# Kernel optimization log

Measured on AMD Instinct MI355X. Metric: run time of the kernel, lower is better.

The kernel has to match this reference:

```python
import jax, jax.numpy as jnp
import numpy as np

N = 100000      # nodes (categories_nums[0])
E = 1600000     # edges
FEAT = 16       # features_num
HID = 32        # hidden
IDE = 16        # id_embed_size
EMB = 8         # embed_size
CAT_MAX = 1000  # categorical vocab (categories_nums[1:])
K = 3           # TAGConv hops (sparse=False)
NC = 2          # num_class
IN_DIM = IDE + 2 * EMB + HID  # 64 -> TAGConv input
EPS = 1e-5


def layer_norm(x, g, b):
    m = jnp.mean(x, axis=-1, keepdims=True)
    v = jnp.mean((x - m) ** 2, axis=-1, keepdims=True)
    return (x - m) * jax.lax.rsqrt(v + EPS) * g + b


def setup_inputs() -> dict:
    key = jax.random.key(0)
    ks = jax.random.split(key, 20)
    s = 0.05
    return {
        "x": jax.random.normal(ks[0], (N, FEAT), jnp.float32),
        "edge_index": jax.random.randint(ks[1], (2, E), 0, N, jnp.int64),
        "edge_weight": jax.random.uniform(ks[2], (E,), jnp.float32),
        "categories_value": jax.random.randint(ks[3], (N, 3), 0, CAT_MAX, jnp.int64),
        "id_table": jax.random.normal(ks[4], (N, IDE), jnp.float32) * s,
        "lin0_id_W": jax.random.normal(ks[5], (IDE, IDE), jnp.float32) * s,
        "lin0_id_b": jnp.zeros((IDE,), jnp.float32),
        "emb1": jax.random.normal(ks[6], (CAT_MAX, EMB), jnp.float32) * s,
        "emb2": jax.random.normal(ks[7], (CAT_MAX, EMB), jnp.float32) * s,
        "lin0_emb_W": jax.random.normal(ks[8], (2 * EMB, 2 * EMB), jnp.float32) * s,
        "lin0_emb_b": jnp.zeros((2 * EMB,), jnp.float32),
        "lin0_W": jax.random.normal(ks[9], (FEAT, HID), jnp.float32) * s,
        "lin0_b": jnp.zeros((HID,), jnp.float32),
        "ln0_g": jnp.ones((IN_DIM,), jnp.float32),
        "ln0_b": jnp.zeros((IN_DIM,), jnp.float32),
        "tag_W": jax.random.normal(ks[10], (K + 1, IN_DIM, HID), jnp.float32) * s,
        "tag_b": jnp.zeros((HID,), jnp.float32),
        "ln1_g": jnp.ones((HID,), jnp.float32),
        "ln1_b": jnp.zeros((HID,), jnp.float32),
        "lin1_W": jax.random.normal(ks[11], (HID, NC), jnp.float32) * s,
        "lin1_b": jnp.zeros((NC,), jnp.float32),
    }


def reference(x, edge_index, edge_weight, categories_value, id_table, lin0_id_W,
              lin0_id_b, emb1, emb2, lin0_emb_W, lin0_emb_b, lin0_W, lin0_b,
              ln0_g, ln0_b, tag_W, tag_b, ln1_g, ln1_b, lin1_W, lin1_b):
    # eval mode: dropouts are identity
    h = jax.nn.elu(x @ lin0_W + lin0_b)                       # [N, HID]
    ide = id_table[categories_value[:, 0]]                    # [N, IDE]
    ide = jax.nn.elu(ide @ lin0_id_W + lin0_id_b)
    er = jnp.concatenate([emb1[categories_value[:, 1]],
                          emb2[categories_value[:, 2]]], axis=1)  # [N, 2*EMB]
    er = jax.nn.elu(er @ lin0_emb_W + lin0_emb_b)
    feat = jnp.concatenate([ide, h, er], axis=1)              # [N, IN_DIM]
    feat = layer_norm(feat, ln0_g, ln0_b)

    # TAGConv: gcn_norm without self-loops, K-hop propagation
    row, col = edge_index[0], edge_index[1]                   # source -> target
    deg = jax.ops.segment_sum(edge_weight, col, num_segments=N)
    dis = jnp.where(deg > 0, deg ** -0.5, 0.0)
    norm = dis[row] * edge_weight * dis[col]                  # [E]

    out = feat @ tag_W[0]                                     # [N, HID]
    xk = feat
    for k in range(1, K + 1):
        xk = jax.ops.segment_sum(xk[row] * norm[:, None], col, num_segments=N)
        out = out + xk @ tag_W[k]
    out = out + tag_b

    out = jax.nn.relu(out)
    out = layer_norm(out, ln1_g, ln1_b)
    out = out @ lin1_W + lin1_b                               # [N, NC]
    return jax.nn.log_softmax(out, axis=-1)
```

## Files before the change

kernel.cpp:

```cpp
#include <hip/hip_runtime.h>
#include <hip/hip_bf16.h>

typedef unsigned short u16;
typedef unsigned int   u32;
typedef unsigned long long u64;
typedef u32 u32x2 __attribute__((ext_vector_type(2)));
typedef u32 u32x4 __attribute__((ext_vector_type(4)));

#define FIX_SCALE 16777216.0f
#define FIX_INV   (1.0f / 16777216.0f)
#define CNT_SHIFT 40
#define DEG_MASK  ((1ULL << CNT_SHIFT) - 1)

__device__ __forceinline__ float b2f(u16 u) { return __uint_as_float(((u32)u) << 16); }
__device__ __forceinline__ u16 f2b(float f) {
    u32 u = __float_as_uint(f);
    return (u16)((u + 0x7FFFu + ((u >> 16) & 1u)) >> 16);
}
__device__ __forceinline__ float elu(float v) { return v > 0.f ? v : expm1f(v); }
__device__ __forceinline__ float ldf(const void* p, size_t i, int f32) {
    return f32 ? ((const float*)p)[i] : b2f(((const u16*)p)[i]);
}
__device__ __forceinline__ float plo(u32 a) { return __uint_as_float(a << 16); }
__device__ __forceinline__ float phi(u32 a) { return __uint_as_float(a & 0xFFFF0000u); }

__global__ void k_flags(const u32* __restrict__ gw, const int* __restrict__ ei,
                        const int* __restrict__ cat, int* __restrict__ flags) {
    if (threadIdx.x == 0 && blockIdx.x == 0) {
        flags[0] = (gw[0] == 0x3F800000u) ? 1 : 0;
        flags[1] = ((ei[1]  | ei[3]  | ei[5]  | ei[7])  == 0) ? 2 : 1;
        flags[2] = ((cat[1] | cat[3] | cat[5] | cat[7]) == 0) ? 2 : 1;
    }
}

__global__ __launch_bounds__(256) void k_feathist(
    const void* __restrict__ x, const int* __restrict__ cat,
    const void* __restrict__ id_table, const void* __restrict__ W_id, const void* __restrict__ b_id,
    const void* __restrict__ emb1, const void* __restrict__ emb2,
    const void* __restrict__ W_emb, const void* __restrict__ b_emb,
    const void* __restrict__ W0, const void* __restrict__ b0,
    const void* __restrict__ g0, const void* __restrict__ bb0,
    const void* __restrict__ tagW,
    float* __restrict__ out_acc, u32* __restrict__ z1, u32* __restrict__ z2, u32* __restrict__ z3,
    const int* __restrict__ ei, const void* __restrict__ ew,
    u64* __restrict__ packed, u16* __restrict__ rank,
    const int* __restrict__ flags, int N, int E, int nbN)
{
    __shared__ float sW0[512];
    __shared__ float sb0[32];
    __shared__ float sWid[256];
    __shared__ float sbid[16];
    __shared__ float sWe[256];
    __shared__ float sbe[16];
    __shared__ float sg[64], sb[64];
    __shared__ float sTt[8192];
    int tid = threadIdx.x;
    int f32 = flags[0], s = flags[1], cs = flags[2];

    int e0 = blockIdx.x * 512 + tid;
    int e1 = e0 + 256;
    u64 old0 = 0, old1 = 0;
    bool h0 = (e0 < E), h1 = (e1 < E);
    const int* colp = ei + (size_t)E * s;
    if (h0) {
        int cdst = colp[(size_t)e0 * s];
        float w = ldf(ew, e0, f32);
        old0 = atomicAdd(&packed[cdst], (1ULL << CNT_SHIFT) | (u64)(w * FIX_SCALE + 0.5f));
    }
    if (h1) {
        int cdst = colp[(size_t)e1 * s];
        float w = ldf(ew, e1, f32);
        old1 = atomicAdd(&packed[cdst], (1ULL << CNT_SHIFT) | (u64)(w * FIX_SCALE + 0.5f));
    }

    if (blockIdx.x < nbN) {
        for (int i = tid; i < 512; i += 256) sW0[i] = ldf(W0, i, f32);
        if (tid < 32) sb0[tid] = ldf(b0, tid, f32);
        sWid[tid] = ldf(W_id, tid, f32);
        if (tid < 16) sbid[tid] = ldf(b_id, tid, f32);
        sWe[tid] = ldf(W_emb, tid, f32);
        if (tid < 16) sbe[tid] = ldf(b_emb, tid, f32);
        if (tid < 64) { sg[tid] = ldf(g0, tid, f32); sb[tid] = ldf(bb0, tid, f32); }
        for (int i = tid; i < 8192; i += 256) {
            int k = i >> 11, r = i & 2047, j = r >> 6, d = r & 63;
            sTt[i] = ldf(tagW, (size_t)k * 2048 + (size_t)d * 32 + j, f32);
        }
        __syncthreads();

        int i = blockIdx.x * 256 + tid;
        if (i < N) {
            size_t cb = (size_t)i * 3 * cs;
            int c0 = cat[cb], c1 = cat[cb + cs], c2 = cat[cb + 2 * cs];
            float f[64];
            {
                float t[16];
                #pragma unroll
                for (int q = 0; q < 16; q++) t[q] = ldf(id_table, (size_t)c0 * 16 + q, f32);
                #pragma unroll
                for (int j = 0; j < 16; j++) {
                    float a = sbid[j];
                    #pragma unroll
                    for (int ff = 0; ff < 16; ff++) a += t[ff] * sWid[ff * 16 + j];
                    f[j] = elu(a);
                }
            }
            {
                float t[16];
                #pragma unroll
                for (int q = 0; q < 16; q++) t[q] = ldf(x, (size_t)i * 16 + q, f32);
                #pragma unroll
                for (int j = 0; j < 32; j++) {
                    float a = sb0[j];
                    #pragma unroll
                    for (int ff = 0; ff < 16; ff++) a += t[ff] * sW0[ff * 32 + j];
                    f[16 + j] = elu(a);
                }
            }
            {
                float t[16];
                #pragma unroll
                for (int q = 0; q < 8; q++) t[q] = ldf(emb1, (size_t)c1 * 8 + q, f32);
                #pragma unroll
                for (int q = 0; q < 8; q++) t[8 + q] = ldf(emb2, (size_t)c2 * 8 + q, f32);
                #pragma unroll
                for (int j = 0; j < 16; j++) {
                    float a = sbe[j];
                    #pragma unroll
                    for (int ff = 0; ff < 16; ff++) a += t[ff] * sWe[ff * 16 + j];
                    f[48 + j] = elu(a);
                }
            }
            float m = 0.f;
            #pragma unroll
            for (int d = 0; d < 64; d++) m += f[d];
            m *= (1.f / 64.f);
            float var = 0.f;
            #pragma unroll
            for (int d = 0; d < 64; d++) { float df = f[d] - m; var += df * df; }
            var *= (1.f / 64.f);
            float rs = rsqrtf(var + 1e-5f);
            #pragma unroll
            for (int d = 0; d < 64; d++) f[d] = (f[d] - m) * rs * sg[d] + sb[d];

            float* oa = out_acc + (size_t)i * 32;
            for (int j = 0; j < 32; j++) {
                float a = 0.f;
                #pragma unroll
                for (int d = 0; d < 64; d++) a += f[d] * sTt[j * 64 + d];
                oa[j] = a;
            }
            #pragma unroll
            for (int k = 1; k <= 3; k++) {
                u32* zp = ((k == 1) ? z1 : (k == 2) ? z2 : z3) + (size_t)i * 16;
                const float* T = sTt + k * 2048;
                for (int j = 0; j < 16; j++) {
                    float a0 = 0.f, a1 = 0.f;
                    #pragma unroll
                    for (int d = 0; d < 64; d++) {
                        a0 += f[d] * T[(2 * j) * 64 + d];
                        a1 += f[d] * T[(2 * j + 1) * 64 + d];
                    }
                    zp[j] = ((u32)f2b(a1) << 16) | f2b(a0);
                }
            }
        }
    }
    if (h0) rank[e0] = (u16)(old0 >> CNT_SHIFT);
    if (h1) rank[e1] = (u16)(old1 >> CNT_SHIFT);
}

__global__ __launch_bounds__(256) void k_scan1(const u64* __restrict__ packed, int* __restrict__ ebuf,
                                               int* __restrict__ bsum, float* __restrict__ dis, int N)
{
    __shared__ int sdat[256];
    int tid = threadIdx.x;
    int i = blockIdx.x * 256 + tid;
    u64 pv = (i < N) ? packed[i] : 0ULL;
    int v = (int)(pv >> CNT_SHIFT);
    sdat[tid] = v;
    __syncthreads();
    for (int off = 1; off < 256; off <<= 1) {
        int t = (tid >= off) ? sdat[tid - off] : 0;
        __syncthreads();
        sdat[tid] += t;
        __syncthreads();
    }
    if (i < N) {
        ebuf[i] = sdat[tid] - v;
        u64 db = pv & DEG_MASK;
        dis[i] = db ? rsqrtf((float)db * FIX_INV) : 0.f;
    }
    if (tid == 255) bsum[blockIdx.x] = sdat[255];
}

__global__ __launch_bounds__(512) void k_scan2(const int* __restrict__ bsum, int* __restrict__ boff, int NB)
{
    __shared__ int sdat[512];
    __shared__ int scarry;
    int tid = threadIdx.x;
    if (tid == 0) scarry = 0;
    __syncthreads();
    for (int base = 0; base < NB; base += 512) {
        int i = base + tid;
        int v = (i < NB) ? bsum[i] : 0;
        sdat[tid] = v;
        __syncthreads();
        for (int off = 1; off < 512; off <<= 1) {
            int t = (tid >= off) ? sdat[tid - off] : 0;
            __syncthreads();
            sdat[tid] += t;
            __syncthreads();
        }
        if (i < NB) boff[i] = scarry + sdat[tid] - v;
        __syncthreads();
        if (tid == 0) scarry += sdat[511];
        __syncthreads();
    }
}

__global__ __launch_bounds__(256) void k_scan3(const int* __restrict__ ebuf, const int* __restrict__ boff,
                                               int* __restrict__ rowptr, int N, int E)
{
    int i = blockIdx.x * 256 + threadIdx.x;
    if (i >= N) return;
    rowptr[i] = boff[blockIdx.x] + ebuf[i];
    if (i == N - 1) rowptr[N] = E;
}

__global__ __launch_bounds__(256) void k_scatter(const int* __restrict__ ei, const void* __restrict__ ew,
                                                 const float* __restrict__ dis, const u16* __restrict__ rank,
                                                 const int* __restrict__ rowptr, int2* __restrict__ csr,
                                                 const int* __restrict__ flags, int E)
{
    int f32 = flags[0], s = flags[1];
    const int* row = ei;
    const int* col = ei + (size_t)E * s;
    int e = blockIdx.x * 256 + threadIdx.x;
    if (e >= E) return;
    int r = row[(size_t)e * s], c = col[(size_t)e * s];
    float nrm = dis[r] * ldf(ew, e, f32) * dis[c];
    csr[rowptr[c] + (int)rank[e]] = make_int2(r, __float_as_int(nrm));
}

template<int ADD>
__global__ __launch_bounds__(256) void k_ahop(
    const u32* __restrict__ zin, const u32* __restrict__ zadd, u32* __restrict__ uout,
    const int* __restrict__ rowptr, const int2* __restrict__ csr, int N)
{
    int tid = threadIdx.x;
    int node = blockIdx.x * 4 + (tid >> 6);
    if (node >= N) return;
    int lane = tid & 63;
    int o = (lane >> 3) & 7;
    int c = lane & 7;
    int start = rowptr[node], end = rowptr[node + 1];

    const u32x2* fin2 = (const u32x2*)zin;
    float v0 = 0.f, v1 = 0.f, v2 = 0.f, v3 = 0.f;
    int e = start;
    for (; e + 16 <= end; e += 16) {
        int2 ma = csr[e + o];
        int2 mb = csr[e + 8 + o];
        u32x2 aa = fin2[(size_t)(u32)ma.x * 8 + c];
        u32x2 ab = fin2[(size_t)(u32)mb.x * 8 + c];
        float wa = __int_as_float(ma.y), wb = __int_as_float(mb.y);
        v0 += plo(aa.x) * wa; v1 += phi(aa.x) * wa; v2 += plo(aa.y) * wa; v3 += phi(aa.y) * wa;
        v0 += plo(ab.x) * wb; v1 += phi(ab.x) * wb; v2 += plo(ab.y) * wb; v3 += phi(ab.y) * wb;
    }
    for (; e < end; e += 8) {
        int ee = e + o;
        int2 m = (ee < end) ? csr[ee] : make_int2(0, 0);
        u32x2 a = fin2[(size_t)(u32)m.x * 8 + c];
        float w = __int_as_float(m.y);
        v0 += plo(a.x) * w; v1 += phi(a.x) * w; v2 += plo(a.y) * w; v3 += phi(a.y) * w;
    }
    v0 += __shfl_xor(v0, 8);  v1 += __shfl_xor(v1, 8);  v2 += __shfl_xor(v2, 8);  v3 += __shfl_xor(v3, 8);
    v0 += __shfl_xor(v0, 16); v1 += __shfl_xor(v1, 16); v2 += __shfl_xor(v2, 16); v3 += __shfl_xor(v3, 16);
    v0 += __shfl_xor(v0, 32); v1 += __shfl_xor(v1, 32); v2 += __shfl_xor(v2, 32); v3 += __shfl_xor(v3, 32);

    if (lane < 8) {
        if (ADD) {
            u32x2 z = ((const u32x2*)zadd)[(size_t)node * 8 + lane];
            v0 += plo(z.x); v1 += phi(z.x); v2 += plo(z.y); v3 += phi(z.y);
        }
        u32x2 pw;
        pw.x = ((u32)f2b(v1) << 16) | f2b(v0);
        pw.y = ((u32)f2b(v3) << 16) | f2b(v2);
        ((u32x2*)uout)[(size_t)node * 8 + lane] = pw;
    }
}

__global__ __launch_bounds__(256) void k_head(
    const float* __restrict__ oacc, const u32* __restrict__ t1,
    const void* __restrict__ tag_b,
    const void* __restrict__ g1, const void* __restrict__ b1,
    const void* __restrict__ W1, const void* __restrict__ bb1,
    void* __restrict__ out, const int* __restrict__ flags, int N)
{
    __shared__ float stb[32], sg[32], sbb[32], sW1[64], sb1v[2];
    int tid = threadIdx.x;
    int f32 = flags[0];
    if (tid < 32) { stb[tid] = ldf(tag_b, tid, f32); sg[tid] = ldf(g1, tid, f32); sbb[tid] = ldf(b1, tid, f32); }
    if (tid < 64) sW1[tid] = ldf(W1, tid, f32);
    if (tid < 2) sb1v[tid] = ldf(bb1, tid, f32);
    __syncthreads();

    int i = blockIdx.x * 256 + tid;
    if (i >= N) return;

    float acc[32];
    const float4* oa4 = (const float4*)(oacc + (size_t)i * 32);
    #pragma unroll
    for (int q = 0; q < 8; q++) {
        float4 t = oa4[q];
        acc[4 * q] = t.x; acc[4 * q + 1] = t.y; acc[4 * q + 2] = t.z; acc[4 * q + 3] = t.w;
    }
    const u32x2* tp = (const u32x2*)t1 + (size_t)i * 8;
    #pragma unroll
    for (int q = 0; q < 8; q++) {
        u32x2 z = tp[q];
        acc[4 * q]     += plo(z.x); acc[4 * q + 1] += phi(z.x);
        acc[4 * q + 2] += plo(z.y); acc[4 * q + 3] += phi(z.y);
    }
    float o[32]; float m = 0.f;
    #pragma unroll
    for (int j = 0; j < 32; j++) { float t = acc[j] + stb[j]; t = t > 0.f ? t : 0.f; o[j] = t; m += t; }
    m *= (1.f / 32.f);
    float var = 0.f;
    #pragma unroll
    for (int j = 0; j < 32; j++) { float d = o[j] - m; var += d * d; }
    var *= (1.f / 32.f);
    float rs = rsqrtf(var + 1e-5f);
    float z0 = sb1v[0], z1 = sb1v[1];
    #pragma unroll
    for (int j = 0; j < 32; j++) {
        float t = (o[j] - m) * rs * sg[j] + sbb[j];
        z0 += t * sW1[2 * j];
        z1 += t * sW1[2 * j + 1];
    }
    float mx = fmaxf(z0, z1);
    float l = mx + logf(expf(z0 - mx) + expf(z1 - mx));
    if (f32) {
        ((float*)out)[(size_t)i * 2]     = z0 - l;
        ((float*)out)[(size_t)i * 2 + 1] = z1 - l;
    } else {
        *((u32*)((u16*)out + (size_t)i * 2)) = ((u32)f2b(z1 - l) << 16) | f2b(z0 - l);
    }
}

extern "C" void kernel_launch(void* const* d_in, const int* in_sizes, int n_in,
                              void* d_out, int out_size, void* d_ws, size_t ws_size,
                              hipStream_t stream)
{
    const void* x        = d_in[0];
    const int*  ei       = (const int*)d_in[1];
    const void* ew       = d_in[2];
    const int*  cat      = (const int*)d_in[3];
    const void* id_table = d_in[4];
    const void* W_id     = d_in[5];
    const void* b_id     = d_in[6];
    const void* emb1     = d_in[7];
    const void* emb2     = d_in[8];
    const void* W_emb    = d_in[9];
    const void* b_emb    = d_in[10];
    const void* W0       = d_in[11];
    const void* b0       = d_in[12];
    const void* g0       = d_in[13];
    const void* bb0      = d_in[14];
    const void* tagW     = d_in[15];
    const void* tag_b    = d_in[16];
    const void* g1       = d_in[17];
    const void* b1       = d_in[18];
    const void* W1       = d_in[19];
    const void* bb1      = d_in[20];

    int N = in_sizes[0] / 16;
    int E = in_sizes[2];
    int nb = (N + 255) / 256;
    int eb = (E + 255) / 256;
    int eb2 = (E + 511) / 512;

    char* ws = (char*)d_ws;
    size_t off = 0;
    int*   flags  = (int*)(ws + off);   off += 256;
    float* oacc   = (float*)(ws + off); off += (size_t)N * 32 * 4;
    u32*   z1     = (u32*)(ws + off);   off += (size_t)N * 16 * 4;
    u32*   z2     = (u32*)(ws + off);   off += (size_t)N * 16 * 4;
    u32*   z3     = (u32*)(ws + off);   off += (size_t)N * 16 * 4;
    u32*   u2     = (u32*)(ws + off);   off += (size_t)N * 16 * 4;
    int2*  csr    = (int2*)(ws + off);  off += (size_t)E * 8;
    int*   rowptr = (int*)(ws + off);   off += ((size_t)N + 1) * 4;
    off = (off + 255) & ~(size_t)255;
    u16*   rank   = (u16*)(ws + off);   off += (size_t)E * 2;
    off = (off + 255) & ~(size_t)255;
    u64*   packed = (u64*)(ws + off);   off += (size_t)N * 8;
    int*   ebuf   = (int*)(ws + off);   off += (size_t)N * 4;
    float* dis    = (float*)(ws + off); off += (size_t)N * 4;
    int*   bsum   = (int*)(ws + off);   off += (size_t)nb * 4;
    int*   boff   = (int*)(ws + off);   off += (size_t)nb * 4;

    hipMemsetAsync(packed, 0, (size_t)N * 8, stream);
    k_flags<<<1, 64, 0, stream>>>((const u32*)g0, ei, cat, flags);

    k_feathist<<<eb2, 256, 0, stream>>>(x, cat, id_table, W_id, b_id, emb1, emb2, W_emb, b_emb,
                                        W0, b0, g0, bb0, tagW, oacc, z1, z2, z3,
                                        ei, ew, packed, rank, flags, N, E, nb);
    k_scan1<<<nb, 256, 0, stream>>>(packed, ebuf, bsum, dis, N);
    k_scan2<<<1, 512, 0, stream>>>(bsum, boff, nb);
    k_scan3<<<nb, 256, 0, stream>>>(ebuf, boff, rowptr, N, E);
    k_scatter<<<eb, 256, 0, stream>>>(ei, ew, dis, rank, rowptr, csr, flags, E);

    int hb = (N + 3) / 4;
    k_ahop<1><<<hb, 256, 0, stream>>>(z3, z2, u2, rowptr, csr, N);
    k_ahop<1><<<hb, 256, 0, stream>>>(u2, z1, z3, rowptr, csr, N);
    k_ahop<0><<<hb, 256, 0, stream>>>(z3, z1, z2, rowptr, csr, N);
    k_head<<<nb, 256, 0, stream>>>(oacc, z2, tag_b, g1, b1, W1, bb1, d_out, flags, N);
}
```

Measured before the change: 365.8 us.

## Split TAG weight projection out of feature kernel into parallel zproj kernel

The per-node 64x128 projection onto the four TAGConv weight matrices moves out of the fused feature/histogram kernel. That kernel now writes a bf16 normalized feature row. A new kernel spreads each node's projection across 8 threads, each handling one hop and one output half, with weights held in padded shared memory. This removes the 32KB shared weight tile and the serial per-thread 8192-FMA loop from the edge-histogram kernel, which should raise occupancy. The cost is an extra launch, an extra round-trip through the bf16 feature buffer, and bf16 rounding of the features before the projection.

Result: slower. 455.4 us (+24.5%).

```diff
diff --git a/kernel.cpp b/kernel.cpp
--- a/kernel.cpp
+++ b/kernel.cpp
@@ -40,8 +40,7 @@
     const void* __restrict__ W_emb, const void* __restrict__ b_emb,
     const void* __restrict__ W0, const void* __restrict__ b0,
     const void* __restrict__ g0, const void* __restrict__ bb0,
-    const void* __restrict__ tagW,
-    float* __restrict__ out_acc, u32* __restrict__ z1, u32* __restrict__ z2, u32* __restrict__ z3,
+    u32* __restrict__ feat,
     const int* __restrict__ ei, const void* __restrict__ ew,
     u64* __restrict__ packed, u16* __restrict__ rank,
     const int* __restrict__ flags, int N, int E, int nbN)
@@ -53,7 +52,6 @@
     __shared__ float sWe[256];
     __shared__ float sbe[16];
     __shared__ float sg[64], sb[64];
-    __shared__ float sTt[8192];
     int tid = threadIdx.x;
     int f32 = flags[0], s = flags[1], cs = flags[2];
 
@@ -81,10 +79,6 @@
         sWe[tid] = ldf(W_emb, tid, f32);
         if (tid < 16) sbe[tid] = ldf(b_emb, tid, f32);
         if (tid < 64) { sg[tid] = ldf(g0, tid, f32); sb[tid] = ldf(bb0, tid, f32); }
-        for (int i = tid; i < 8192; i += 256) {
-            int k = i >> 11, r = i & 2047, j = r >> 6, d = r & 63;
-            sTt[i] = ldf(tagW, (size_t)k * 2048 + (size_t)d * 32 + j, f32);
-        }
         __syncthreads();
 
         int i = blockIdx.x * 256 + tid;
@@ -142,31 +136,64 @@
             #pragma unroll
             for (int d = 0; d < 64; d++) f[d] = (f[d] - m) * rs * sg[d] + sb[d];
 
-            float* oa = out_acc + (size_t)i * 32;
-            for (int j = 0; j < 32; j++) {
-                float a = 0.f;
-                #pragma unroll
-                for (int d = 0; d < 64; d++) a += f[d] * sTt[j * 64 + d];
-                oa[j] = a;
-            }
+            u32* fp = feat + (size_t)i * 32;
             #pragma unroll
-            for (int k = 1; k <= 3; k++) {
-                u32* zp = ((k == 1) ? z1 : (k == 2) ? z2 : z3) + (size_t)i * 16;
-                const float* T = sTt + k * 2048;
-                for (int j = 0; j < 16; j++) {
-                    float a0 = 0.f, a1 = 0.f;
-                    #pragma unroll
-                    for (int d = 0; d < 64; d++) {
-                        a0 += f[d] * T[(2 * j) * 64 + d];
-                        a1 += f[d] * T[(2 * j + 1) * 64 + d];
-                    }
-                    zp[j] = ((u32)f2b(a1) << 16) | f2b(a0);
-                }
-            }
+            for (int q = 0; q < 32; q++) fp[q] = ((u32)f2b(f[2 * q + 1]) << 16) | f2b(f[2 * q]);
         }
     }
     if (h0) rank[e0] = (u16)(old0 >> CNT_SHIFT);
     if (h1) rank[e1] = (u16)(old1 >> CNT_SHIFT);
+}
+
+__global__ __launch_bounds__(256) void k_zproj(
+    const u32* __restrict__ feat, const void* __restrict__ tagW,
+    float* __restrict__ oacc, u32* __restrict__ z1, u32* __restrict__ z2, u32* __restrict__ z3,
+    const int* __restrict__ flags, int N)
+{
+    __shared__ float sT[4 * 2056];
+    int tid = threadIdx.x;
+    int f32 = flags[0];
+    for (int i = tid; i < 8192; i += 256) {
+        int k = i >> 11, r = i & 2047;
+        sT[k * 2056 + r] = ldf(tagW, i, f32);
+    }
+    __syncthreads();
+
+    int nblk = blockIdx.x * 32 + (tid >> 3);
+    if (nblk >= N) return;
+    int sub = tid & 7, kk = sub >> 1, h = sub & 1;
+
+    const u32x4* fp4 = (const u32x4*)(feat + (size_t)nblk * 32);
+    float f[64];
+    #pragma unroll
+    for (int q = 0; q < 8; q++) {
+        u32x4 a = fp4[q];
+        f[8 * q + 0] = plo(a.x); f[8 * q + 1] = phi(a.x);
+        f[8 * q + 2] = plo(a.y); f[8 * q + 3] = phi(a.y);
+        f[8 * q + 4] = plo(a.z); f[8 * q + 5] = phi(a.z);
+        f[8 * q + 6] = plo(a.w); f[8 * q + 7] = phi(a.w);
+    }
+
+    float o[16];
+    #pragma unroll
+    for (int j = 0; j < 16; j++) o[j] = 0.f;
+    const float* T = sT + kk * 2056 + h * 16;
+    #pragma unroll 4
+    for (int d = 0; d < 64; d++) {
+        float fd = f[d];
+        #pragma unroll
+        for (int j = 0; j < 16; j++) o[j] += fd * T[d * 32 + j];
+    }
+
+    if (kk == 0) {
+        float4* op = (float4*)(oacc + (size_t)nblk * 32 + h * 16);
+        #pragma unroll
+        for (int q = 0; q < 4; q++) op[q] = make_float4(o[4 * q], o[4 * q + 1], o[4 * q + 2], o[4 * q + 3]);
+    } else {
+        u32* zp = ((kk == 1) ? z1 : (kk == 2) ? z2 : z3) + (size_t)nblk * 16 + h * 8;
+        #pragma unroll
+        for (int jj = 0; jj < 8; jj++) zp[jj] = ((u32)f2b(o[2 * jj + 1]) << 16) | f2b(o[2 * jj]);
+    }
 }
 
 __global__ __launch_bounds__(256) void k_scan1(const u64* __restrict__ packed, int* __restrict__ ebuf,
@@ -379,11 +406,13 @@
     int nb = (N + 255) / 256;
     int eb = (E + 255) / 256;
     int eb2 = (E + 511) / 512;
+    int zb = (N + 31) / 32;
 
     char* ws = (char*)d_ws;
     size_t off = 0;
     int*   flags  = (int*)(ws + off);   off += 256;
     float* oacc   = (float*)(ws + off); off += (size_t)N * 32 * 4;
+    u32*   feat   = (u32*)(ws + off);   off += (size_t)N * 32 * 4;
     u32*   z1     = (u32*)(ws + off);   off += (size_t)N * 16 * 4;
     u32*   z2     = (u32*)(ws + off);   off += (size_t)N * 16 * 4;
     u32*   z3     = (u32*)(ws + off);   off += (size_t)N * 16 * 4;
@@ -403,8 +432,10 @@
     k_flags<<<1, 64, 0, stream>>>((const u32*)g0, ei, cat, flags);
 
     k_feathist<<<eb2, 256, 0, stream>>>(x, cat, id_table, W_id, b_id, emb1, emb2, W_emb, b_emb,
-                                        W0, b0, g0, bb0, tagW, oacc, z1, z2, z3,
+                                        W0, b0, g0, bb0, feat,
                                         ei, ew, packed, rank, flags, N, E, nb);
+    k_zproj<<<zb, 256, 0, stream>>>(feat, tagW, oacc, z1, z2, z3, flags, N);
+
     k_scan1<<<nb, 256, 0, stream>>>(packed, ebuf, bsum, dis, N);
     k_scan2<<<1, 512, 0, stream>>>(bsum, boff, nb);
     k_scan3<<<nb, 256, 0, stream>>>(ebuf, boff, rowptr, N, E);
```

## Rebalance fused feature/histogram kernel: 16 edges per thread, all blocks compute nodes

Applied to the files above, without the earlier changes.

The fused feature-transform and degree-histogram kernel now launches about as many blocks as node tiles, with each thread handling 16 edges instead of 2. All 16 edge atomics are issued together before the dense projection, so their latency can overlap with the matmul work. The TAG weight matrix is kept in its natural row layout, the projection is restructured as an outer product with 32 accumulators, and outputs are written with vector stores. In exchange, each thread holds many more live registers (f[64], o[32], 16 pending atomics), which may lower occupancy.

Measured after the change: 479.0 us. +31.0%, slower.

```diff
diff --git a/kernel.cpp b/kernel.cpp
--- a/kernel.cpp
+++ b/kernel.cpp
@@ -41,10 +41,10 @@
     const void* __restrict__ W0, const void* __restrict__ b0,
     const void* __restrict__ g0, const void* __restrict__ bb0,
     const void* __restrict__ tagW,
-    float* __restrict__ out_acc, u32* __restrict__ z1, u32* __restrict__ z2, u32* __restrict__ z3,
+    float* __restrict__ oacc, u32* __restrict__ z1, u32* __restrict__ z2, u32* __restrict__ z3,
     const int* __restrict__ ei, const void* __restrict__ ew,
     u64* __restrict__ packed, u16* __restrict__ rank,
-    const int* __restrict__ flags, int N, int E, int nbN)
+    const int* __restrict__ flags, int N, int E)
 {
     __shared__ float sW0[512];
     __shared__ float sb0[32];
@@ -53,120 +53,132 @@
     __shared__ float sWe[256];
     __shared__ float sbe[16];
     __shared__ float sg[64], sb[64];
-    __shared__ float sTt[8192];
+    __shared__ float sT[4 * 2048];
     int tid = threadIdx.x;
     int f32 = flags[0], s = flags[1], cs = flags[2];
 
-    int e0 = blockIdx.x * 512 + tid;
-    int e1 = e0 + 256;
-    u64 old0 = 0, old1 = 0;
-    bool h0 = (e0 < E), h1 = (e1 < E);
+    for (int i = tid; i < 512; i += 256) sW0[i] = ldf(W0, i, f32);
+    if (tid < 32) sb0[tid] = ldf(b0, tid, f32);
+    sWid[tid] = ldf(W_id, tid, f32);
+    if (tid < 16) sbid[tid] = ldf(b_id, tid, f32);
+    sWe[tid] = ldf(W_emb, tid, f32);
+    if (tid < 16) sbe[tid] = ldf(b_emb, tid, f32);
+    if (tid < 64) { sg[tid] = ldf(g0, tid, f32); sb[tid] = ldf(bb0, tid, f32); }
+    for (int i = tid; i < 8192; i += 256) sT[i] = ldf(tagW, i, f32);
+    __syncthreads();
+
+    int i = blockIdx.x * 256 + tid;
+    bool node = (i < N);
+    float f[64];
+    if (node) {
+        size_t cb = (size_t)i * 3 * cs;
+        int c0 = cat[cb], c1 = cat[cb + cs], c2 = cat[cb + 2 * cs];
+        {
+            float t[16];
+            #pragma unroll
+            for (int q = 0; q < 16; q++) t[q] = ldf(id_table, (size_t)c0 * 16 + q, f32);
+            #pragma unroll
+            for (int j = 0; j < 16; j++) {
+                float a = sbid[j];
+                #pragma unroll
+                for (int ff = 0; ff < 16; ff++) a += t[ff] * sWid[ff * 16 + j];
+                f[j] = elu(a);
+            }
+        }
+        {
+            float t[16];
+            #pragma unroll
+            for (int q = 0; q < 16; q++) t[q] = ldf(x, (size_t)i * 16 + q, f32);
+            #pragma unroll
+            for (int j = 0; j < 32; j++) {
+                float a = sb0[j];
+                #pragma unroll
+                for (int ff = 0; ff < 16; ff++) a += t[ff] * sW0[ff * 32 + j];
+                f[16 + j] = elu(a);
+            }
+        }
+        {
+            float t[16];
+            #pragma unroll
+            for (int q = 0; q < 8; q++) t[q] = ldf(emb1, (size_t)c1 * 8 + q, f32);
+            #pragma unroll
+            for (int q = 0; q < 8; q++) t[8 + q] = ldf(emb2, (size_t)c2 * 8 + q, f32);
+            #pragma unroll
+            for (int j = 0; j < 16; j++) {
+                float a = sbe[j];
+                #pragma unroll
+                for (int ff = 0; ff < 16; ff++) a += t[ff] * sWe[ff * 16 + j];
+                f[48 + j] = elu(a);
+            }
+        }
+        float m = 0.f;
+        #pragma unroll
+        for (int d = 0; d < 64; d++) m += f[d];
+        m *= (1.f / 64.f);
+        float var = 0.f;
+        #pragma unroll
+        for (int d = 0; d < 64; d++) { float df = f[d] - m; var += df * df; }
+        var *= (1.f / 64.f);
+        float rs = rsqrtf(var + 1e-5f);
+        #pragma unroll
+        for (int d = 0; d < 64; d++) f[d] = (f[d] - m) * rs * sg[d] + sb[d];
+    }
+
+    int ebase = blockIdx.x * 4096 + tid;
     const int* colp = ei + (size_t)E * s;
-    if (h0) {
-        int cdst = colp[(size_t)e0 * s];
-        float w = ldf(ew, e0, f32);
-        old0 = atomicAdd(&packed[cdst], (1ULL << CNT_SHIFT) | (u64)(w * FIX_SCALE + 0.5f));
-    }
-    if (h1) {
-        int cdst = colp[(size_t)e1 * s];
-        float w = ldf(ew, e1, f32);
-        old1 = atomicAdd(&packed[cdst], (1ULL << CNT_SHIFT) | (u64)(w * FIX_SCALE + 0.5f));
-    }
-
-    if (blockIdx.x < nbN) {
-        for (int i = tid; i < 512; i += 256) sW0[i] = ldf(W0, i, f32);
-        if (tid < 32) sb0[tid] = ldf(b0, tid, f32);
-        sWid[tid] = ldf(W_id, tid, f32);
-        if (tid < 16) sbid[tid] = ldf(b_id, tid, f32);
-        sWe[tid] = ldf(W_emb, tid, f32);
-        if (tid < 16) sbe[tid] = ldf(b_emb, tid, f32);
-        if (tid < 64) { sg[tid] = ldf(g0, tid, f32); sb[tid] = ldf(bb0, tid, f32); }
-        for (int i = tid; i < 8192; i += 256) {
-            int k = i >> 11, r = i & 2047, j = r >> 6, d = r & 63;
-            sTt[i] = ldf(tagW, (size_t)k * 2048 + (size_t)d * 32 + j, f32);
-        }
-        __syncthreads();
-
-        int i = blockIdx.x * 256 + tid;
-        if (i < N) {
-            size_t cb = (size_t)i * 3 * cs;
-            int c0 = cat[cb], c1 = cat[cb + cs], c2 = cat[cb + 2 * cs];
-            float f[64];
-            {
-                float t[16];
-                #pragma unroll
-                for (int q = 0; q < 16; q++) t[q] = ldf(id_table, (size_t)c0 * 16 + q, f32);
-                #pragma unroll
-                for (int j = 0; j < 16; j++) {
-                    float a = sbid[j];
-                    #pragma unroll
-                    for (int ff = 0; ff < 16; ff++) a += t[ff] * sWid[ff * 16 + j];
-                    f[j] = elu(a);
+    int cd[16]; float wv[16];
+    #pragma unroll
+    for (int k = 0; k < 16; k++) {
+        int e = ebase + (k << 8);
+        if (e < E) { cd[k] = colp[(size_t)e * s]; wv[k] = ldf(ew, e, f32); }
+    }
+    u64 olds[16];
+    #pragma unroll
+    for (int k = 0; k < 16; k++) {
+        int e = ebase + (k << 8);
+        if (e < E)
+            olds[k] = atomicAdd(&packed[cd[k]],
+                                (1ULL << CNT_SHIFT) | (u64)(wv[k] * FIX_SCALE + 0.5f));
+    }
+
+    if (node) {
+        #pragma unroll
+        for (int p = 0; p < 4; p++) {
+            float o[32];
+            #pragma unroll
+            for (int j = 0; j < 32; j++) o[j] = 0.f;
+            const float* T = sT + p * 2048;
+            #pragma unroll
+            for (int d = 0; d < 64; d++) {
+                float fd = f[d];
+                #pragma unroll
+                for (int j = 0; j < 32; j++) o[j] += fd * T[d * 32 + j];
+            }
+            if (p == 0) {
+                float4* op = (float4*)(oacc + (size_t)i * 32);
+                #pragma unroll
+                for (int q = 0; q < 8; q++)
+                    op[q] = make_float4(o[4 * q], o[4 * q + 1], o[4 * q + 2], o[4 * q + 3]);
+            } else {
+                u32* zp = ((p == 1) ? z1 : (p == 2) ? z2 : z3) + (size_t)i * 16;
+                #pragma unroll
+                for (int q = 0; q < 4; q++) {
+                    u32x4 pw;
+                    pw.x = ((u32)f2b(o[8 * q + 1]) << 16) | f2b(o[8 * q + 0]);
+                    pw.y = ((u32)f2b(o[8 * q + 3]) << 16) | f2b(o[8 * q + 2]);
+                    pw.z = ((u32)f2b(o[8 * q + 5]) << 16) | f2b(o[8 * q + 4]);
+                    pw.w = ((u32)f2b(o[8 * q + 7]) << 16) | f2b(o[8 * q + 6]);
+                    ((u32x4*)zp)[q] = pw;
                 }
             }
-            {
-                float t[16];
-                #pragma unroll
-                for (int q = 0; q < 16; q++) t[q] = ldf(x, (size_t)i * 16 + q, f32);
-                #pragma unroll
-                for (int j = 0; j < 32; j++) {
-                    float a = sb0[j];
-                    #pragma unroll
-                    for (int ff = 0; ff < 16; ff++) a += t[ff] * sW0[ff * 32 + j];
-                    f[16 + j] = elu(a);
-                }
-            }
-            {
-                float t[16];
-                #pragma unroll
-                for (int q = 0; q < 8; q++) t[q] = ldf(emb1, (size_t)c1 * 8 + q, f32);
-                #pragma unroll
-                for (int q = 0; q < 8; q++) t[8 + q] = ldf(emb2, (size_t)c2 * 8 + q, f32);
-                #pragma unroll
-                for (int j = 0; j < 16; j++) {
-                    float a = sbe[j];
-                    #pragma unroll
-                    for (int ff = 0; ff < 16; ff++) a += t[ff] * sWe[ff * 16 + j];
-                    f[48 + j] = elu(a);
-                }
-            }
-            float m = 0.f;
-            #pragma unroll
-            for (int d = 0; d < 64; d++) m += f[d];
-            m *= (1.f / 64.f);
-            float var = 0.f;
-            #pragma unroll
-            for (int d = 0; d < 64; d++) { float df = f[d] - m; var += df * df; }
-            var *= (1.f / 64.f);
-            float rs = rsqrtf(var + 1e-5f);
-            #pragma unroll
-            for (int d = 0; d < 64; d++) f[d] = (f[d] - m) * rs * sg[d] + sb[d];
-
-            float* oa = out_acc + (size_t)i * 32;
-            for (int j = 0; j < 32; j++) {
-                float a = 0.f;
-                #pragma unroll
-                for (int d = 0; d < 64; d++) a += f[d] * sTt[j * 64 + d];
-                oa[j] = a;
-            }
-            #pragma unroll
-            for (int k = 1; k <= 3; k++) {
-                u32* zp = ((k == 1) ? z1 : (k == 2) ? z2 : z3) + (size_t)i * 16;
-                const float* T = sTt + k * 2048;
-                for (int j = 0; j < 16; j++) {
-                    float a0 = 0.f, a1 = 0.f;
-                    #pragma unroll
-                    for (int d = 0; d < 64; d++) {
-                        a0 += f[d] * T[(2 * j) * 64 + d];
-                        a1 += f[d] * T[(2 * j + 1) * 64 + d];
-                    }
-                    zp[j] = ((u32)f2b(a1) << 16) | f2b(a0);
-                }
-            }
-        }
-    }
-    if (h0) rank[e0] = (u16)(old0 >> CNT_SHIFT);
-    if (h1) rank[e1] = (u16)(old1 >> CNT_SHIFT);
+        }
+    }
+
+    #pragma unroll
+    for (int k = 0; k < 16; k++) {
+        int e = ebase + (k << 8);
+        if (e < E) rank[e] = (u16)(olds[k] >> CNT_SHIFT);
+    }
 }
 
 __global__ __launch_bounds__(256) void k_scan1(const u64* __restrict__ packed, int* __restrict__ ebuf,
@@ -378,7 +390,8 @@
     int E = in_sizes[2];
     int nb = (N + 255) / 256;
     int eb = (E + 255) / 256;
-    int eb2 = (E + 511) / 512;
+    int fb = (E + 4095) / 4096;
+    if (fb < nb) fb = nb;
 
     char* ws = (char*)d_ws;
     size_t off = 0;
@@ -402,9 +415,10 @@
     hipMemsetAsync(packed, 0, (size_t)N * 8, stream);
     k_flags<<<1, 64, 0, stream>>>((const u32*)g0, ei, cat, flags);
 
-    k_feathist<<<eb2, 256, 0, stream>>>(x, cat, id_table, W_id, b_id, emb1, emb2, W_emb, b_emb,
-                                        W0, b0, g0, bb0, tagW, oacc, z1, z2, z3,
-                                        ei, ew, packed, rank, flags, N, E, nb);
+    k_feathist<<<fb, 256, 0, stream>>>(x, cat, id_table, W_id, b_id, emb1, emb2, W_emb, b_emb,
+                                       W0, b0, g0, bb0, tagW, oacc, z1, z2, z3,
+                                       ei, ew, packed, rank, flags, N, E);
+
     k_scan1<<<nb, 256, 0, stream>>>(packed, ebuf, bsum, dis, N);
     k_scan2<<<1, 512, 0, stream>>>(bsum, boff, nb);
     k_scan3<<<nb, 256, 0, stream>>>(ebuf, boff, rowptr, N, E);
```

## Split node feature work across 8 lanes per node with shuffle-based layernorm

Applied to the files above, without the earlier changes.

The fused feature/histogram kernel now processes 32 nodes per block with 8 threads per node instead of one thread per node over the first N/256 blocks. Inputs and embedding rows are staged in shared memory, layernorm statistics are reduced with warp shuffles, and each lane computes one 16-wide slice of one of the four TAG projections, writing vectorized stores. This spreads the heavy per-node 64x128 matmul across all edge blocks instead of a few threads, reducing register pressure and serialization. In exchange, every block reloads the full 8K weight table into shared memory and the matmul issues many lane shuffles.

Result: slower. 395.5 us (+8.1%).

```diff
diff --git a/kernel.cpp b/kernel.cpp
--- a/kernel.cpp
+++ b/kernel.cpp
@@ -41,130 +41,169 @@
     const void* __restrict__ W0, const void* __restrict__ b0,
     const void* __restrict__ g0, const void* __restrict__ bb0,
     const void* __restrict__ tagW,
-    float* __restrict__ out_acc, u32* __restrict__ z1, u32* __restrict__ z2, u32* __restrict__ z3,
+    float* __restrict__ oacc, u32* __restrict__ z1, u32* __restrict__ z2, u32* __restrict__ z3,
     const int* __restrict__ ei, const void* __restrict__ ew,
     u64* __restrict__ packed, u16* __restrict__ rank,
-    const int* __restrict__ flags, int N, int E, int nbN)
+    const int* __restrict__ flags, int N, int E)
 {
     __shared__ float sW0[512];
-    __shared__ float sb0[32];
+    __shared__ float sb0v[32];
     __shared__ float sWid[256];
     __shared__ float sbid[16];
     __shared__ float sWe[256];
     __shared__ float sbe[16];
     __shared__ float sg[64], sb[64];
-    __shared__ float sTt[8192];
+    __shared__ float sT[4 * 2056];
+    __shared__ float sx[32 * 17];
+    __shared__ float sid[32 * 17];
+    __shared__ float se[32 * 17];
+    __shared__ int   scat[96];
     int tid = threadIdx.x;
     int f32 = flags[0], s = flags[1], cs = flags[2];
 
     int e0 = blockIdx.x * 512 + tid;
     int e1 = e0 + 256;
-    u64 old0 = 0, old1 = 0;
     bool h0 = (e0 < E), h1 = (e1 < E);
     const int* colp = ei + (size_t)E * s;
-    if (h0) {
-        int cdst = colp[(size_t)e0 * s];
-        float w = ldf(ew, e0, f32);
-        old0 = atomicAdd(&packed[cdst], (1ULL << CNT_SHIFT) | (u64)(w * FIX_SCALE + 0.5f));
-    }
-    if (h1) {
-        int cdst = colp[(size_t)e1 * s];
-        float w = ldf(ew, e1, f32);
-        old1 = atomicAdd(&packed[cdst], (1ULL << CNT_SHIFT) | (u64)(w * FIX_SCALE + 0.5f));
-    }
-
-    if (blockIdx.x < nbN) {
-        for (int i = tid; i < 512; i += 256) sW0[i] = ldf(W0, i, f32);
-        if (tid < 32) sb0[tid] = ldf(b0, tid, f32);
-        sWid[tid] = ldf(W_id, tid, f32);
-        if (tid < 16) sbid[tid] = ldf(b_id, tid, f32);
-        sWe[tid] = ldf(W_emb, tid, f32);
-        if (tid < 16) sbe[tid] = ldf(b_emb, tid, f32);
-        if (tid < 64) { sg[tid] = ldf(g0, tid, f32); sb[tid] = ldf(bb0, tid, f32); }
-        for (int i = tid; i < 8192; i += 256) {
-            int k = i >> 11, r = i & 2047, j = r >> 6, d = r & 63;
-            sTt[i] = ldf(tagW, (size_t)k * 2048 + (size_t)d * 32 + j, f32);
-        }
-        __syncthreads();
-
-        int i = blockIdx.x * 256 + tid;
-        if (i < N) {
-            size_t cb = (size_t)i * 3 * cs;
-            int c0 = cat[cb], c1 = cat[cb + cs], c2 = cat[cb + 2 * cs];
-            float f[64];
-            {
-                float t[16];
-                #pragma unroll
-                for (int q = 0; q < 16; q++) t[q] = ldf(id_table, (size_t)c0 * 16 + q, f32);
-                #pragma unroll
-                for (int j = 0; j < 16; j++) {
-                    float a = sbid[j];
-                    #pragma unroll
-                    for (int ff = 0; ff < 16; ff++) a += t[ff] * sWid[ff * 16 + j];
-                    f[j] = elu(a);
-                }
+    int cd0 = 0, cd1 = 0; float w0 = 0.f, w1 = 0.f;
+    if (h0) { cd0 = colp[(size_t)e0 * s]; w0 = ldf(ew, e0, f32); }
+    if (h1) { cd1 = colp[(size_t)e1 * s]; w1 = ldf(ew, e1, f32); }
+
+    int nb0 = blockIdx.x * 32;
+    int nv = N - nb0; if (nv > 32) nv = 32; if (nv < 0) nv = 0;
+    for (int i = tid; i < 512; i += 256) sW0[i] = ldf(W0, i, f32);
+    if (tid < 32) sb0v[tid] = ldf(b0, tid, f32);
+    sWid[tid] = ldf(W_id, tid, f32);
+    if (tid < 16) sbid[tid] = ldf(b_id, tid, f32);
+    sWe[tid] = ldf(W_emb, tid, f32);
+    if (tid < 16) sbe[tid] = ldf(b_emb, tid, f32);
+    if (tid < 64) { sg[tid] = ldf(g0, tid, f32); sb[tid] = ldf(bb0, tid, f32); }
+    for (int i = tid; i < 8192; i += 256) {
+        int k = i >> 11, r = i & 2047;
+        sT[k * 2056 + r] = ldf(tagW, i, f32);
+    }
+    for (int i = tid; i < nv * 16; i += 256)
+        sx[(i >> 4) * 17 + (i & 15)] = ldf(x, (size_t)nb0 * 16 + i, f32);
+    if (tid < nv * 3) scat[tid] = cat[((size_t)nb0 * 3 + tid) * cs];
+    __syncthreads();
+
+    for (int i = tid; i < nv * 16; i += 256) {
+        int nl = i >> 4, q = i & 15;
+        sid[nl * 17 + q] = ldf(id_table, (size_t)scat[nl * 3] * 16 + q, f32);
+        se[nl * 17 + q] = (q < 8) ? ldf(emb1, (size_t)scat[nl * 3 + 1] * 8 + q, f32)
+                                  : ldf(emb2, (size_t)scat[nl * 3 + 2] * 8 + (q - 8), f32);
+    }
+    __syncthreads();
+
+    u64 old0 = 0, old1 = 0;
+    if (h0) old0 = atomicAdd(&packed[cd0], (1ULL << CNT_SHIFT) | (u64)(w0 * FIX_SCALE + 0.5f));
+    if (h1) old1 = atomicAdd(&packed[cd1], (1ULL << CNT_SHIFT) | (u64)(w1 * FIX_SCALE + 0.5f));
+
+    int nl = tid >> 3, sub = tid & 7;
+    bool node = (nl < nv);
+    float f0 = 0.f, f1 = 0.f, f2 = 0.f, f3 = 0.f, f4 = 0.f, f5 = 0.f, f6 = 0.f, f7 = 0.f;
+    if (node) {
+        const float* xin = sx + nl * 17;
+        const float* iin = sid + nl * 17;
+        const float* ein = se + nl * 17;
+        {
+            float a0 = sbid[2 * sub], a1 = sbid[2 * sub + 1];
+            #pragma unroll
+            for (int ff = 0; ff < 16; ff++) {
+                float t = iin[ff];
+                a0 += t * sWid[ff * 16 + 2 * sub];
+                a1 += t * sWid[ff * 16 + 2 * sub + 1];
             }
-            {
-                float t[16];
-                #pragma unroll
-                for (int q = 0; q < 16; q++) t[q] = ldf(x, (size_t)i * 16 + q, f32);
-                #pragma unroll
-                for (int j = 0; j < 32; j++) {
-                    float a = sb0[j];
-                    #pragma unroll
-                    for (int ff = 0; ff < 16; ff++) a += t[ff] * sW0[ff * 32 + j];
-                    f[16 + j] = elu(a);
-                }
+            f0 = elu(a0); f1 = elu(a1);
+        }
+        {
+            float a0 = sb0v[4 * sub], a1 = sb0v[4 * sub + 1];
+            float a2 = sb0v[4 * sub + 2], a3 = sb0v[4 * sub + 3];
+            #pragma unroll
+            for (int ff = 0; ff < 16; ff++) {
+                float t = xin[ff];
+                a0 += t * sW0[ff * 32 + 4 * sub];
+                a1 += t * sW0[ff * 32 + 4 * sub + 1];
+                a2 += t * sW0[ff * 32 + 4 * sub + 2];
+                a3 += t * sW0[ff * 32 + 4 * sub + 3];
             }
-            {
-                float t[16];
-                #pragma unroll
-                for (int q = 0; q < 8; q++) t[q] = ldf(emb1, (size_t)c1 * 8 + q, f32);
-                #pragma unroll
-                for (int q = 0; q < 8; q++) t[8 + q] = ldf(emb2, (size_t)c2 * 8 + q, f32);
-                #pragma unroll
-                for (int j = 0; j < 16; j++) {
-                    float a = sbe[j];
-                    #pragma unroll
-                    for (int ff = 0; ff < 16; ff++) a += t[ff] * sWe[ff * 16 + j];
-                    f[48 + j] = elu(a);
-                }
+            f2 = elu(a0); f3 = elu(a1); f4 = elu(a2); f5 = elu(a3);
+        }
+        {
+            float a0 = sbe[2 * sub], a1 = sbe[2 * sub + 1];
+            #pragma unroll
+            for (int ff = 0; ff < 16; ff++) {
+                float t = ein[ff];
+                a0 += t * sWe[ff * 16 + 2 * sub];
+                a1 += t * sWe[ff * 16 + 2 * sub + 1];
             }
-            float m = 0.f;
-            #pragma unroll
-            for (int d = 0; d < 64; d++) m += f[d];
-            m *= (1.f / 64.f);
-            float var = 0.f;
-            #pragma unroll
-            for (int d = 0; d < 64; d++) { float df = f[d] - m; var += df * df; }
-            var *= (1.f / 64.f);
-            float rs = rsqrtf(var + 1e-5f);
-            #pragma unroll
-            for (int d = 0; d < 64; d++) f[d] = (f[d] - m) * rs * sg[d] + sb[d];
-
-            float* oa = out_acc + (size_t)i * 32;
-            for (int j = 0; j < 32; j++) {
-                float a = 0.f;
-                #pragma unroll
-                for (int d = 0; d < 64; d++) a += f[d] * sTt[j * 64 + d];
-                oa[j] = a;
+            f6 = elu(a0); f7 = elu(a1);
+        }
+    }
+    float sm = f0 + f1 + f2 + f3 + f4 + f5 + f6 + f7;
+    sm += __shfl_xor(sm, 1); sm += __shfl_xor(sm, 2); sm += __shfl_xor(sm, 4);
+    float m = sm * (1.f / 64.f);
+    float d0 = f0 - m, d1 = f1 - m, d2 = f2 - m, d3 = f3 - m;
+    float d4 = f4 - m, d5 = f5 - m, d6 = f6 - m, d7 = f7 - m;
+    float vq = d0 * d0 + d1 * d1 + d2 * d2 + d3 * d3 + d4 * d4 + d5 * d5 + d6 * d6 + d7 * d7;
+    vq += __shfl_xor(vq, 1); vq += __shfl_xor(vq, 2); vq += __shfl_xor(vq, 4);
+    float rs = rsqrtf(vq * (1.f / 64.f) + 1e-5f);
+    f0 = d0 * rs * sg[2 * sub] + sb[2 * sub];
+    f1 = d1 * rs * sg[2 * sub + 1] + sb[2 * sub + 1];
+    f2 = d2 * rs * sg[16 + 4 * sub] + sb[16 + 4 * sub];
+    f3 = d3 * rs * sg[16 + 4 * sub + 1] + sb[16 + 4 * sub + 1];
+    f4 = d4 * rs * sg[16 + 4 * sub + 2] + sb[16 + 4 * sub + 2];
+    f5 = d5 * rs * sg[16 + 4 * sub + 3] + sb[16 + 4 * sub + 3];
+    f6 = d6 * rs * sg[48 + 2 * sub] + sb[48 + 2 * sub];
+    f7 = d7 * rs * sg[48 + 2 * sub + 1] + sb[48 + 2 * sub + 1];
+
+    {
+        int kk = sub >> 1, h = sub & 1;
+        int lbase = (tid & 56);
+        float o[16];
+        #pragma unroll
+        for (int j = 0; j < 16; j++) o[j] = 0.f;
+        const float* T = sT + kk * 2056 + h * 16;
+        #pragma unroll
+        for (int d = 0; d < 64; d++) {
+            float fd;
+            if (d < 16)      fd = __shfl((d & 1) ? f1 : f0, lbase + (d >> 1));
+            else if (d < 48) {
+                int dd = d - 16;
+                int r = dd & 3;
+                fd = __shfl(r == 0 ? f2 : r == 1 ? f3 : r == 2 ? f4 : f5, lbase + (dd >> 2));
+            } else {
+                int dd = d - 48;
+                fd = __shfl((dd & 1) ? f7 : f6, lbase + (dd >> 1));
             }
             #pragma unroll
-            for (int k = 1; k <= 3; k++) {
-                u32* zp = ((k == 1) ? z1 : (k == 2) ? z2 : z3) + (size_t)i * 16;
-                const float* T = sTt + k * 2048;
-                for (int j = 0; j < 16; j++) {
-                    float a0 = 0.f, a1 = 0.f;
-                    #pragma unroll
-                    for (int d = 0; d < 64; d++) {
-                        a0 += f[d] * T[(2 * j) * 64 + d];
-                        a1 += f[d] * T[(2 * j + 1) * 64 + d];
-                    }
-                    zp[j] = ((u32)f2b(a1) << 16) | f2b(a0);
-                }
+            for (int j = 0; j < 16; j++) o[j] += fd * T[d * 32 + j];
+        }
+        if (node) {
+            int gnode = nb0 + nl;
+            if (kk == 0) {
+                float4* op = (float4*)(oacc + (size_t)gnode * 32 + h * 16);
+                op[0] = make_float4(o[0], o[1], o[2], o[3]);
+                op[1] = make_float4(o[4], o[5], o[6], o[7]);
+                op[2] = make_float4(o[8], o[9], o[10], o[11]);
+                op[3] = make_float4(o[12], o[13], o[14], o[15]);
+            } else {
+                u32* zp = ((kk == 1) ? z1 : (kk == 2) ? z2 : z3) + (size_t)gnode * 16 + h * 8;
+                u32x4 pa, pb;
+                pa.x = ((u32)f2b(o[1]) << 16) | f2b(o[0]);
+                pa.y = ((u32)f2b(o[3]) << 16) | f2b(o[2]);
+                pa.z = ((u32)f2b(o[5]) << 16) | f2b(o[4]);
+                pa.w = ((u32)f2b(o[7]) << 16) | f2b(o[6]);
+                pb.x = ((u32)f2b(o[9]) << 16) | f2b(o[8]);
+                pb.y = ((u32)f2b(o[11]) << 16) | f2b(o[10]);
+                pb.z = ((u32)f2b(o[13]) << 16) | f2b(o[12]);
+                pb.w = ((u32)f2b(o[15]) << 16) | f2b(o[14]);
+                ((u32x4*)zp)[0] = pa;
+                ((u32x4*)zp)[1] = pb;
             }
         }
     }
+
     if (h0) rank[e0] = (u16)(old0 >> CNT_SHIFT);
     if (h1) rank[e1] = (u16)(old1 >> CNT_SHIFT);
 }
@@ -379,6 +418,8 @@
     int nb = (N + 255) / 256;
     int eb = (E + 255) / 256;
     int eb2 = (E + 511) / 512;
+    int nb32 = (N + 31) / 32;
+    int fb = eb2 > nb32 ? eb2 : nb32;
 
     char* ws = (char*)d_ws;
     size_t off = 0;
@@ -402,9 +443,10 @@
     hipMemsetAsync(packed, 0, (size_t)N * 8, stream);
     k_flags<<<1, 64, 0, stream>>>((const u32*)g0, ei, cat, flags);
 
-    k_feathist<<<eb2, 256, 0, stream>>>(x, cat, id_table, W_id, b_id, emb1, emb2, W_emb, b_emb,
-                                        W0, b0, g0, bb0, tagW, oacc, z1, z2, z3,
-                                        ei, ew, packed, rank, flags, N, E, nb);
+    k_feathist<<<fb, 256, 0, stream>>>(x, cat, id_table, W_id, b_id, emb1, emb2, W_emb, b_emb,
+                                       W0, b0, g0, bb0, tagW, oacc, z1, z2, z3,
+                                       ei, ew, packed, rank, flags, N, E);
+
     k_scan1<<<nb, 256, 0, stream>>>(packed, ebuf, bsum, dis, N);
     k_scan2<<<1, 512, 0, stream>>>(bsum, boff, nb);
     k_scan3<<<nb, 256, 0, stream>>>(ebuf, boff, rowptr, N, E);
```
